# Kernel tuning notes

Measured on AMD Instinct MI355X. Metric: run time of the kernel, lower is better.

Reference implementation:

```python
import jax, jax.numpy as jnp
import numpy as np

B, S, D, H = 4, 8192, 1024, 16   # batch, seq, in_feature==out_feature, num_heads
SCALE = (D // H) ** -0.5          # torch: (key.size(-1) // num_heads) ** -0.5 = 64**-0.5
EPS = 1e-5


def setup_inputs() -> dict:
    key = jax.random.key(0)
    ks = jax.random.split(key, 8)
    return {
        "query": jax.random.normal(ks[0], (B, S, D), dtype=jnp.float32),
        "key": jax.random.normal(ks[1], (B, S, D), dtype=jnp.float32),
        "value": jax.random.normal(ks[2], (B, S, D), dtype=jnp.float32),
        "wq": jax.random.normal(ks[3], (D, D), dtype=jnp.float32) * 0.02,
        "wk": jax.random.normal(ks[4], (D, D), dtype=jnp.float32) * 0.02,
        "wv": jax.random.normal(ks[5], (D, D), dtype=jnp.float32) * 0.02,
        "w_final": jax.random.normal(ks[6], (D, D), dtype=jnp.float32) * 0.02,
        "b_final": jnp.zeros((D,), dtype=jnp.float32),
        "gamma": jnp.ones((D,), dtype=jnp.float32),
        "beta": jnp.zeros((D,), dtype=jnp.float32),
    }


def reference(query, key, value, wq, wk, wv, w_final, b_final, gamma, beta):
    residual = query
    # projections: [B, S, D]
    q = jnp.matmul(query, wq)
    k = jnp.matmul(key, wk)
    v = jnp.matmul(value, wv)
    # faithful to source: view splits the SEQUENCE dim into H blocks -> [B*H, S/H, D]
    q = q.reshape(B * H, S // H, D)
    k = k.reshape(B * H, S // H, D)
    v = v.reshape(B * H, S // H, D)
    # scaled dot-product attention per block (no mask, dropout=0)
    scores = jnp.einsum("bqd,bkd->bqk", q, k) * SCALE   # [B*H, S/H, S/H]
    attention = jax.nn.softmax(scores, axis=2)
    context = jnp.einsum("bqk,bkd->bqd", attention, v)   # [B*H, S/H, D]
    context = context.reshape(B, S, D)                   # dim_per_head*H == D
    output = jnp.matmul(context, w_final.T) + b_final
    # layernorm(residual + output)
    x = residual + output
    mean = jnp.mean(x, axis=-1, keepdims=True)
    var = jnp.var(x, axis=-1, keepdims=True)
    out = (x - mean) * jax.lax.rsqrt(var + EPS) * gamma + beta
    return (out, attention)
```

## Files before the change

kernel.cpp:

```cpp
#include <hip/hip_runtime.h>

typedef unsigned short u16;
typedef __bf16 bf16x8 __attribute__((ext_vector_type(8)));
typedef float floatx4 __attribute__((ext_vector_type(4)));
typedef u16 u16x8 __attribute__((ext_vector_type(8)));


__device__ __forceinline__ u16 f2bf(float f) {
  union { float f; unsigned u; } x; x.f = f;
  unsigned r = x.u + 0x7FFFu + ((x.u >> 16) & 1u);
  return (u16)(r >> 16);
}

__device__ __forceinline__ void async16(const u16* g, u16* l) {
  __builtin_amdgcn_global_load_lds((const __attribute__((address_space(1))) void*)g,
                                   (__attribute__((address_space(3))) void*)l,
                                   16, 0, 0);
}

__global__ __launch_bounds__(256) void wconv_t(const float* __restrict__ wq,
                                               const float* __restrict__ wk,
                                               const float* __restrict__ wv,
                                               u16* __restrict__ dst0) {
  const float* src = blockIdx.z == 0 ? wq : (blockIdx.z == 1 ? wk : wv);
  u16* dst = dst0 + (size_t)blockIdx.z * 1024 * 1024;
  __shared__ float t[32][33];
  int k0 = blockIdx.y * 32, n0 = blockIdx.x * 32;
  int tid = threadIdx.x;
  int row = tid >> 3, c4 = (tid & 7) * 4;
  float4 v = *(const float4*)&src[(size_t)(k0 + row) * 1024 + n0 + c4];
  t[row][c4 + 0] = v.x; t[row][c4 + 1] = v.y; t[row][c4 + 2] = v.z; t[row][c4 + 3] = v.w;
  __syncthreads();
  ushort4 u;
  u.x = f2bf(t[c4 + 0][row]);
  u.y = f2bf(t[c4 + 1][row]);
  u.z = f2bf(t[c4 + 2][row]);
  u.w = f2bf(t[c4 + 3][row]);
  *(ushort4*)&dst[(size_t)(n0 + row) * 1024 + k0 + c4] = u;
}

__global__ __launch_bounds__(256) void wconv(const float* __restrict__ w, u16* __restrict__ dst) {
  size_t i = ((size_t)blockIdx.x * 256 + threadIdx.x) * 4;
  float4 v = *(const float4*)&w[i];
  ushort4 u; u.x = f2bf(v.x); u.y = f2bf(v.y); u.z = f2bf(v.z); u.w = f2bf(v.w);
  *(ushort4*)&dst[i] = u;
}

__global__ __launch_bounds__(256) void cast_bf16(const float* __restrict__ q,
                                                 const float* __restrict__ k,
                                                 const float* __restrict__ v,
                                                 u16* __restrict__ dst0) {
  const float* src = blockIdx.z == 0 ? q : (blockIdx.z == 1 ? k : v);
  u16* dst = dst0 + (size_t)blockIdx.z * 33554432;
  size_t i = ((size_t)blockIdx.x * 256 + threadIdx.x) * 8;
  float4 a = *(const float4*)&src[i];
  float4 b = *(const float4*)&src[i + 4];
  u16x8 o;
  o[0] = f2bf(a.x); o[1] = f2bf(a.y); o[2] = f2bf(a.z); o[3] = f2bf(a.w);
  o[4] = f2bf(b.x); o[5] = f2bf(b.y); o[6] = f2bf(b.z); o[7] = f2bf(b.w);
  *(u16x8*)&dst[i] = o;
}

__global__ __launch_bounds__(256) void transpose_v(const u16* __restrict__ V,
                                                   u16* __restrict__ Vt) {
  __shared__ u16 t[64][65];
  const u16* src = V + (size_t)blockIdx.z * 512 * 1024;
  u16* dst = Vt + (size_t)blockIdx.z * 1024 * 512;
  int s0 = blockIdx.y * 64, d0 = blockIdx.x * 64;
  int tid = threadIdx.x;
#pragma unroll
  for (int i = 0; i < 4; ++i) {
    int row = i * 16 + (tid >> 4);
    int c4 = (tid & 15) * 4;
    ushort4 v = *(const ushort4*)&src[(size_t)(s0 + row) * 1024 + d0 + c4];
    t[row][c4 + 0] = v.x; t[row][c4 + 1] = v.y; t[row][c4 + 2] = v.z; t[row][c4 + 3] = v.w;
  }
  __syncthreads();
#pragma unroll
  for (int i = 0; i < 4; ++i) {
    int row = i * 16 + (tid >> 4);
    int c4 = (tid & 15) * 4;
    ushort4 u;
    u.x = t[c4 + 0][row]; u.y = t[c4 + 1][row]; u.z = t[c4 + 2][row]; u.w = t[c4 + 3][row];
    *(ushort4*)&dst[(size_t)(d0 + row) * 512 + s0 + c4] = u;
  }
}

template <int OMODE>
__global__ __launch_bounds__(256) void gemm_bt(
    const u16* __restrict__ Ap, const u16* __restrict__ Bp, void* __restrict__ Cp,
    int K, int lda, int ldb, int ldc,
    int sA, int sB, int sC,
    const float* __restrict__ res, const float* __restrict__ bias, float scale) {
  __shared__ u16 Asm[128 * 32];
  __shared__ u16 Bsm[128 * 32];

  const int tid = threadIdx.x;
  const int wave = tid >> 6, lane = tid & 63;
  const int wm = wave >> 1, wn = wave & 1;
  const int quad = lane >> 4, r16 = lane & 15;

  const unsigned gx = gridDim.x, gy = gridDim.y;
  const unsigned nwg = gx * gy * gridDim.z;
  unsigned bid = (blockIdx.z * gy + blockIdx.y) * gx + blockIdx.x;
  unsigned nb = (bid & 7u) * (nwg >> 3) + (bid >> 3);
  const unsigned bx = nb & (gx - 1u);
  nb >>= __builtin_ctz(gx);
  const unsigned by = nb & (gy - 1u);
  nb >>= __builtin_ctz(gy);
  const unsigned bz = nb;

  const unsigned m0 = by * 128u;
  const unsigned n0 = bx * 128u;

  const u16* Ab = Ap + (size_t)bz * (unsigned)sA;
  const u16* Bb = Bp + (size_t)bz * (unsigned)sB;

  const int srow = lane >> 2;
  const int scol = (lane & 3) * 8;
  const u16* ga = Ab + (size_t)((m0 + wave * 16 + srow) * (unsigned)lda + scol);
  const u16* gb = Bb + (size_t)((n0 + wave * 16 + srow) * (unsigned)ldb + scol);
  const size_t stepA = (size_t)64 * (unsigned)lda;
  const size_t stepB = (size_t)64 * (unsigned)ldb;
  u16* la = &Asm[wave * 512];
  u16* lb = &Bsm[wave * 512];

  floatx4 acc[4][4] = {};

  for (int k0 = 0; k0 < K; k0 += 32) {
    async16(ga, la);
    async16(ga + stepA, la + 2048);
    async16(gb, lb);
    async16(gb + stepB, lb + 2048);
    ga += 32;
    gb += 32;
    __syncthreads();

    bf16x8 af[4], bfr[4];
#pragma unroll
    for (int i = 0; i < 4; ++i)
      af[i] = *(const bf16x8*)&Asm[(wm * 64 + i * 16 + r16) * 32 + quad * 8];
#pragma unroll
    for (int j = 0; j < 4; ++j)
      bfr[j] = *(const bf16x8*)&Bsm[(wn * 64 + j * 16 + r16) * 32 + quad * 8];
#pragma unroll
    for (int i = 0; i < 4; ++i)
#pragma unroll
      for (int j = 0; j < 4; ++j)
        acc[i][j] = __builtin_amdgcn_mfma_f32_16x16x32_bf16(af[i], bfr[j], acc[i][j], 0, 0, 0);
    __syncthreads();
  }

#pragma unroll
  for (int i = 0; i < 4; ++i) {
    unsigned row = m0 + wm * 64 + i * 16 + quad * 4;
#pragma unroll
    for (int j = 0; j < 4; ++j) {
      unsigned col = n0 + wn * 64 + j * 16 + r16;
#pragma unroll
      for (int r = 0; r < 4; ++r) {
        unsigned idx = (row + r) * (unsigned)ldc + col;
        if constexpr (OMODE == 0) {
          ((u16*)Cp)[(size_t)bz * (unsigned)sC + idx] = f2bf(acc[i][j][r]);
        } else if constexpr (OMODE == 1) {
          ((float*)Cp)[(size_t)bz * (unsigned)sC + idx] = acc[i][j][r] * scale;
        } else {
          float xv = acc[i][j][r] + bias[col] + res[idx];
          ((float*)Cp)[idx] = xv;
        }
      }
    }
  }
}

__global__ __launch_bounds__(256) void softmax_k(float* __restrict__ attn,
                                                 u16* __restrict__ Pb) {
  size_t row = (size_t)blockIdx.x * 4 + (threadIdx.x >> 6);
  int lane = threadIdx.x & 63;
  float* p = attn + row * 512 + lane * 8;
  float4 a = *(const float4*)p;
  float4 b = *(const float4*)(p + 4);
  float m = fmaxf(fmaxf(fmaxf(a.x, a.y), fmaxf(a.z, a.w)),
                  fmaxf(fmaxf(b.x, b.y), fmaxf(b.z, b.w)));
#pragma unroll
  for (int off = 32; off >= 1; off >>= 1) m = fmaxf(m, __shfl_xor(m, off));
  float e[8];
  e[0] = __expf(a.x - m); e[1] = __expf(a.y - m); e[2] = __expf(a.z - m); e[3] = __expf(a.w - m);
  e[4] = __expf(b.x - m); e[5] = __expf(b.y - m); e[6] = __expf(b.z - m); e[7] = __expf(b.w - m);
  float s = e[0] + e[1] + e[2] + e[3] + e[4] + e[5] + e[6] + e[7];
#pragma unroll
  for (int off = 32; off >= 1; off >>= 1) s += __shfl_xor(s, off);
  float inv = 1.0f / s;
  float o[8];
#pragma unroll
  for (int i = 0; i < 8; ++i) o[i] = e[i] * inv;
  float4 oa, ob;
  oa.x = o[0]; oa.y = o[1]; oa.z = o[2]; oa.w = o[3];
  ob.x = o[4]; ob.y = o[5]; ob.z = o[6]; ob.w = o[7];
  *(float4*)p = oa;
  *(float4*)(p + 4) = ob;
  u16x8 pb;
#pragma unroll
  for (int i = 0; i < 8; ++i) pb[i] = f2bf(o[i]);
  *(u16x8*)&Pb[row * 512 + lane * 8] = pb;
}

__global__ __launch_bounds__(256) void layernorm_k(const float* __restrict__ x,
                                                   const float* __restrict__ gamma,
                                                   const float* __restrict__ beta,
                                                   float* __restrict__ out) {
  size_t row = blockIdx.x;
  int tid = threadIdx.x, lane = tid & 63, wave = tid >> 6;
  float4 v = *(const float4*)&x[row * 1024 + tid * 4];
  float s = v.x + v.y + v.z + v.w;
  float q = v.x * v.x + v.y * v.y + v.z * v.z + v.w * v.w;
#pragma unroll
  for (int off = 32; off >= 1; off >>= 1) {
    s += __shfl_xor(s, off);
    q += __shfl_xor(q, off);
  }
  __shared__ float ss[4], qq[4];
  if (lane == 0) { ss[wave] = s; qq[wave] = q; }
  __syncthreads();
  s = ss[0] + ss[1] + ss[2] + ss[3];
  q = qq[0] + qq[1] + qq[2] + qq[3];
  float mean = s * (1.0f / 1024.0f);
  float var = q * (1.0f / 1024.0f) - mean * mean;
  float rstd = rsqrtf(var + 1e-5f);
  float4 g = *(const float4*)&gamma[tid * 4];
  float4 be = *(const float4*)&beta[tid * 4];
  float4 o;
  o.x = (v.x - mean) * rstd * g.x + be.x;
  o.y = (v.y - mean) * rstd * g.y + be.y;
  o.z = (v.z - mean) * rstd * g.z + be.z;
  o.w = (v.w - mean) * rstd * g.w + be.w;
  *(float4*)&out[row * 1024 + tid * 4] = o;
}

extern "C" void kernel_launch(void* const* d_in, const int* in_sizes, int n_in,
                              void* d_out, int out_size, void* d_ws, size_t ws_size,
                              hipStream_t stream) {
  const float* query = (const float*)d_in[0];
  const float* key   = (const float*)d_in[1];
  const float* value = (const float*)d_in[2];
  const float* wq    = (const float*)d_in[3];
  const float* wk    = (const float*)d_in[4];
  const float* wv    = (const float*)d_in[5];
  const float* wfin  = (const float*)d_in[6];
  const float* bfin  = (const float*)d_in[7];
  const float* gamma = (const float*)d_in[8];
  const float* beta  = (const float*)d_in[9];

  char* ws = (char*)d_ws;
  u16* WQT = (u16*)ws;
  u16* WKT = WQT + 1024 * 1024;
  u16* WVT = WKT + 1024 * 1024;
  u16* WF  = WVT + 1024 * 1024;
  u16* Qin = (u16*)(ws + 8388608);
  u16* Kin = Qin + 33554432;
  u16* Vin = Kin + 33554432;
  u16* Qb  = (u16*)(ws + 209715200);
  u16* Kb  = Qb + 33554432;
  u16* Vb  = Qin;
  u16* VTb = Kin;
  u16* Pb  = Vin;
  u16* CTX = Qin;
  float* X = (float*)(ws + 209715200);

  float* out  = (float*)d_out;
  float* attn = out + 33554432;

  dim3 blk(256);

  wconv_t<<<dim3(32, 32, 3), blk, 0, stream>>>(wq, wk, wv, WQT);
  wconv<<<dim3(1024), blk, 0, stream>>>(wfin, WF);
  cast_bf16<<<dim3(16384, 1, 3), blk, 0, stream>>>(query, key, value, Qin);

  gemm_bt<0><<<dim3(8, 256, 1), blk, 0, stream>>>(Qin, WQT, Qb, 1024, 1024, 1024, 1024,
                                                  0, 0, 0, nullptr, nullptr, 1.0f);
  gemm_bt<0><<<dim3(8, 256, 1), blk, 0, stream>>>(Kin, WKT, Kb, 1024, 1024, 1024, 1024,
                                                  0, 0, 0, nullptr, nullptr, 1.0f);
  gemm_bt<0><<<dim3(8, 256, 1), blk, 0, stream>>>(Vin, WVT, Vb, 1024, 1024, 1024, 1024,
                                                  0, 0, 0, nullptr, nullptr, 1.0f);

  transpose_v<<<dim3(16, 8, 64), blk, 0, stream>>>(Vb, VTb);

  gemm_bt<1><<<dim3(4, 4, 64), blk, 0, stream>>>(Qb, Kb, attn, 1024, 1024, 1024, 512,
                                                 524288, 524288, 262144,
                                                 nullptr, nullptr, 0.125f);

  softmax_k<<<dim3(8192), blk, 0, stream>>>(attn, Pb);

  gemm_bt<0><<<dim3(8, 4, 64), blk, 0, stream>>>(Pb, VTb, CTX, 512, 512, 512, 1024,
                                                 262144, 524288, 524288,
                                                 nullptr, nullptr, 1.0f);

  gemm_bt<2><<<dim3(8, 256, 1), blk, 0, stream>>>(CTX, WF, X, 1024, 1024, 1024, 1024,
                                                  0, 0, 0, query, bfin, 1.0f);

  layernorm_k<<<dim3(32768), blk, 0, stream>>>(X, gamma, beta, out);
}
```

Measured before the change: 1.179 ms.

## Double-buffer LDS tiles in gemm_bt to overlap global loads with MFMA

Splits the shared-memory A/B tiles into two ping-pong buffers so the next K-slice is fetched asynchronously into one buffer while MFMAs consume the other. This removes one barrier per iteration and hides global-load latency behind compute. LDS per block doubles, and launch_bounds now requests 3 blocks per CU, which may constrain registers. The loop assumes K/32 is even.

Result: faster. 1.113 ms (-5.6%).

```diff
diff --git a/kernel.cpp b/kernel.cpp
--- a/kernel.cpp
+++ b/kernel.cpp
@@ -87,13 +87,15 @@
 }
 
 template <int OMODE>
-__global__ __launch_bounds__(256) void gemm_bt(
+__global__ __launch_bounds__(256, 3) void gemm_bt(
     const u16* __restrict__ Ap, const u16* __restrict__ Bp, void* __restrict__ Cp,
     int K, int lda, int ldb, int ldc,
     int sA, int sB, int sC,
     const float* __restrict__ res, const float* __restrict__ bias, float scale) {
-  __shared__ u16 Asm[128 * 32];
-  __shared__ u16 Bsm[128 * 32];
+  __shared__ u16 A0[128 * 32];
+  __shared__ u16 B0[128 * 32];
+  __shared__ u16 A1[128 * 32];
+  __shared__ u16 B1[128 * 32];
 
   const int tid = threadIdx.x;
   const int wave = tid >> 6, lane = tid & 63;
@@ -122,34 +124,52 @@
   const u16* gb = Bb + (size_t)((n0 + wave * 16 + srow) * (unsigned)ldb + scol);
   const size_t stepA = (size_t)64 * (unsigned)lda;
   const size_t stepB = (size_t)64 * (unsigned)ldb;
-  u16* la = &Asm[wave * 512];
-  u16* lb = &Bsm[wave * 512];
+  u16* la0 = &A0[wave * 512];
+  u16* lb0 = &B0[wave * 512];
+  u16* la1 = &A1[wave * 512];
+  u16* lb1 = &B1[wave * 512];
 
   floatx4 acc[4][4] = {};
 
-  for (int k0 = 0; k0 < K; k0 += 32) {
-    async16(ga, la);
-    async16(ga + stepA, la + 2048);
-    async16(gb, lb);
-    async16(gb + stepB, lb + 2048);
-    ga += 32;
-    gb += 32;
-    __syncthreads();
-
+  auto compute = [&](const u16* AS, const u16* BS) {
     bf16x8 af[4], bfr[4];
 #pragma unroll
     for (int i = 0; i < 4; ++i)
-      af[i] = *(const bf16x8*)&Asm[(wm * 64 + i * 16 + r16) * 32 + quad * 8];
+      af[i] = *(const bf16x8*)&AS[(wm * 64 + i * 16 + r16) * 32 + quad * 8];
 #pragma unroll
     for (int j = 0; j < 4; ++j)
-      bfr[j] = *(const bf16x8*)&Bsm[(wn * 64 + j * 16 + r16) * 32 + quad * 8];
+      bfr[j] = *(const bf16x8*)&BS[(wn * 64 + j * 16 + r16) * 32 + quad * 8];
 #pragma unroll
     for (int i = 0; i < 4; ++i)
 #pragma unroll
       for (int j = 0; j < 4; ++j)
         acc[i][j] = __builtin_amdgcn_mfma_f32_16x16x32_bf16(af[i], bfr[j], acc[i][j], 0, 0, 0);
+  };
+
+  const int nt = K >> 5;
+
+  async16(ga, la0); async16(ga + stepA, la0 + 2048);
+  async16(gb, lb0); async16(gb + stepB, lb0 + 2048);
+  ga += 32; gb += 32;
+  __syncthreads();
+
+  for (int t = 1; t + 1 < nt; t += 2) {
+    async16(ga, la1); async16(ga + stepA, la1 + 2048);
+    async16(gb, lb1); async16(gb + stepB, lb1 + 2048);
+    ga += 32; gb += 32;
+    compute(A0, B0);
     __syncthreads();
-  }
+    async16(ga, la0); async16(ga + stepA, la0 + 2048);
+    async16(gb, lb0); async16(gb + stepB, lb0 + 2048);
+    ga += 32; gb += 32;
+    compute(A1, B1);
+    __syncthreads();
+  }
+  async16(ga, la1); async16(ga + stepA, la1 + 2048);
+  async16(gb, lb1); async16(gb + stepB, lb1 + 2048);
+  compute(A0, B0);
+  __syncthreads();
+  compute(A1, B1);
 
 #pragma unroll
   for (int i = 0; i < 4; ++i) {
```
